# Kernel optimization log

Hardware: AMD Instinct MI355X
Metric: run time of the kernel (lower is better)

Reference implementation:

```python
import jax, jax.numpy as jnp
import numpy as np

EPS = 1e-5

def bn_relu(x, g, b):
    # MinkowskiBatchNorm (training mode: batch statistics over points) + ReLU
    mu = x.mean(0)
    var = jnp.var(x, axis=0)
    return jax.nn.relu((x - mu) * jax.lax.rsqrt(var + EPS) * g + b)

def setup_inputs() -> dict:
    key = jax.random.key(0)
    ks = jax.random.split(key, 8)
    N, C, H, K, M = 131072, 128, 2, 27, 2
    x = jax.random.normal(ks[0], (N, C), jnp.float32)
    nbr = jax.random.randint(ks[1], (N, K), 0, N, dtype=jnp.int32)  # kernel map
    Wv = jax.random.normal(ks[2], (C, C * H), jnp.float32) * 0.05   # 1x1 conv for v
    gv, bv = jnp.ones(C * H), jnp.zeros(C * H)
    Wq = jax.random.normal(ks[3], (K, C, 1), jnp.float32) * 0.05    # 3x3x3 conv for q (vec_dim=1)
    gq, bq = jnp.ones(1), jnp.zeros(1)
    cb = jax.random.normal(ks[4], (M, K, C * H), jnp.float32) * 0.05  # M channelwise conv kernels
    Wout = jax.random.normal(ks[5], (C * H, C), jnp.float32) * 0.05   # out 1x1 conv
    go, bo = jnp.ones(C), jnp.zeros(C)
    return dict(x=x, nbr=nbr, Wv=Wv, gv=gv, bv=bv, Wq=Wq, gq=gq, bq=bq,
                cb=cb, Wout=Wout, go=go, bo=bo)

def reference(x, nbr, Wv, gv, bv, Wq, gq, bq, cb, Wout, go, bo):
    N = x.shape[0]
    res = x  # inplanes == planes -> no downsample
    v = bn_relu(x @ Wv, gv, bv)                      # [N, 2C]
    nbrT = nbr.T                                     # [K, N]

    # q: sparse 3x3x3 conv planes -> vec_dim=1, scan over the 27 kernel offsets
    def qbody(acc, inp):
        idx, w = inp                                 # idx [N], w [C,1]
        return acc + x[idx] @ w, None
    q, _ = jax.lax.scan(qbody, jnp.zeros((N, Wq.shape[2]), x.dtype), (nbrT, Wq))
    q = bn_relu(q, gq, bq)                           # [N, 1]

    # choice: channelwise conv of channel-broadcast q with each codebook kernel,
    # summed over channels (vec_dim=1) -> equivalent to q_nbr @ kernel_channel_sums.
    # Codebook kernels have requires_grad=False in this path.
    ksum = jax.lax.stop_gradient(cb).sum(-1)         # [M, K]
    qn = q[:, 0][nbr]                                # [N, K]
    choice = jax.nn.softmax(qn @ ksum.T, axis=-1)    # [N, M], temp = 1

    # routed channelwise convs on v: sum_m choice[:,m] * chanconv_m(v)
    # fused as per-offset mix of the M kernels by choice.
    def obody(acc, inp):
        idx, wk = inp                                # idx [N], wk [M, 2C]
        return acc + v[idx] * (choice @ wk), None
    out, _ = jax.lax.scan(obody, jnp.zeros_like(v), (nbrT, jnp.swapaxes(cb, 0, 1)))

    out = bn_relu(out @ Wout, go, bo)                # [N, C]
    return out + res
```

## Files before the change

### kernel.cpp

```cpp
#include <hip/hip_runtime.h>
#include <math.h>

#define EPSV 1e-5f

__device__ __forceinline__ unsigned short f2bf(float f) {
    unsigned u = __float_as_uint(f);
    u += 0x7fffu + ((u >> 16) & 1u);
    return (unsigned short)(u >> 16);
}
__device__ __forceinline__ float bf2f(unsigned short h) {
    return __uint_as_float(((unsigned)h) << 16);
}

__global__ __launch_bounds__(256)
void prep_kernel(const float* __restrict__ Wv, const float* __restrict__ Wq,
                 const float* __restrict__ cb,
                 float* __restrict__ wcat, float* __restrict__ ksum,
                 float* __restrict__ stats)
{
    const long gid = (long)blockIdx.x * 256 + threadIdx.x;
    if (gid < 128L * 384) {
        const int r = (int)(gid / 384);
        const int c = (int)(gid % 384);
        float v = 0.f;
        if (c < 256)      v = Wv[r * 256 + c];
        else if (c < 283) v = Wq[(c - 256) * 128 + r];
        wcat[gid] = v;
    }
    if (gid < 1024) stats[gid] = 0.f;
    if (gid < 64) {
        float s = 0.f;
        if (gid < 27) { const float* p = cb + gid * 256; for (int c = 0; c < 256; ++c) s += p[c]; }
        else if (gid >= 32 && gid < 59) { const float* p = cb + (27 + (gid - 32)) * 256; for (int c = 0; c < 256; ++c) s += p[c]; }
        ksum[gid] = s;
    }
}

__global__ __launch_bounds__(256)
void gemm1_kernel(const float* __restrict__ A,
                  const float* __restrict__ B,
                  unsigned short* __restrict__ t1b,
                  float* __restrict__ y)
{
    __shared__ float As[16][132];
    __shared__ float Bs[16][132];
    const int tid = threadIdx.x;
    const int tx = tid & 15;
    const int ty = tid >> 4;
    const long rowBase = (long)blockIdx.y * 128;
    const int  colBase = blockIdx.x * 128;

    float acc[8][8];
    #pragma unroll
    for (int i = 0; i < 8; ++i)
        #pragma unroll
        for (int j = 0; j < 8; ++j) acc[i][j] = 0.f;

    const int ar = tid >> 2;
    const int ak = (tid & 3) * 4;
    const int bk = tid >> 5;
    const int bc = (tid & 31) * 4;

    for (int k0 = 0; k0 < 128; k0 += 16) {
        #pragma unroll
        for (int p = 0; p < 2; ++p) {
            const int r = ar + p * 64;
            const float4 av = *(const float4*)(A + (rowBase + r) * 128 + (k0 + ak));
            As[ak + 0][r] = av.x;
            As[ak + 1][r] = av.y;
            As[ak + 2][r] = av.z;
            As[ak + 3][r] = av.w;
        }
        #pragma unroll
        for (int p = 0; p < 2; ++p) {
            const int kk = bk + p * 8;
            *(float4*)&Bs[kk][bc] = *(const float4*)(B + (long)(k0 + kk) * 384 + (colBase + bc));
        }
        __syncthreads();
        #pragma unroll
        for (int kk = 0; kk < 16; ++kk) {
            const float4 a0 = *(const float4*)&As[kk][ty * 8];
            const float4 a1 = *(const float4*)&As[kk][ty * 8 + 4];
            const float4 b0 = *(const float4*)&Bs[kk][tx * 4];
            const float4 b1 = *(const float4*)&Bs[kk][64 + tx * 4];
            const float a[8] = {a0.x, a0.y, a0.z, a0.w, a1.x, a1.y, a1.z, a1.w};
            const float b[8] = {b0.x, b0.y, b0.z, b0.w, b1.x, b1.y, b1.z, b1.w};
            #pragma unroll
            for (int i = 0; i < 8; ++i)
                #pragma unroll
                for (int j = 0; j < 8; ++j)
                    acc[i][j] = fmaf(a[i], b[j], acc[i][j]);
        }
        __syncthreads();
    }

    if (colBase < 256) {
        #pragma unroll
        for (int i = 0; i < 8; ++i) {
            const long r = rowBase + ty * 8 + i;
            ushort4 u0, u1;
            u0.x = f2bf(acc[i][0]); u0.y = f2bf(acc[i][1]); u0.z = f2bf(acc[i][2]); u0.w = f2bf(acc[i][3]);
            u1.x = f2bf(acc[i][4]); u1.y = f2bf(acc[i][5]); u1.z = f2bf(acc[i][6]); u1.w = f2bf(acc[i][7]);
            *(ushort4*)(t1b + r * 256 + colBase + tx * 4)      = u0;
            *(ushort4*)(t1b + r * 256 + colBase + 64 + tx * 4) = u1;
        }
    } else {
        #pragma unroll
        for (int i = 0; i < 8; ++i) {
            const long r = rowBase + ty * 8 + i;
            #pragma unroll
            for (int j = 0; j < 8; ++j) {
                const int c = ((j < 4) ? (tx * 4 + j) : (64 + tx * 4 + (j - 4)));
                if (c < 27) y[r * 27 + c] = acc[i][j];
            }
        }
    }
}

__global__ __launch_bounds__(256)
void stats_t1(const unsigned short* __restrict__ t1b, float* __restrict__ stats)
{
    const int c = threadIdx.x;
    const long r0 = (long)blockIdx.x * 256;
    float s = 0.f, s2 = 0.f;
    #pragma unroll 4
    for (int r = 0; r < 256; ++r) {
        const float v = bf2f(t1b[(r0 + r) * 256 + c]);
        s += v; s2 += v * v;
    }
    atomicAdd(&stats[c], s);
    atomicAdd(&stats[256 + c], s2);
}

__global__ __launch_bounds__(256)
void qpre_kernel(const float* __restrict__ y, const int* __restrict__ nbr,
                 float* __restrict__ qpre, float* __restrict__ stats)
{
    __shared__ int snbr[256 * 27];
    __shared__ float red[8];
    const int tid = threadIdx.x;
    const long base = (long)blockIdx.x * 256;
    for (int j = tid; j < 256 * 27; j += 256) snbr[j] = nbr[base * 27 + j];
    __syncthreads();
    float q = 0.f;
    #pragma unroll
    for (int k = 0; k < 27; ++k) {
        const int idx = snbr[tid * 27 + k];
        q += y[(long)idx * 27 + k];
    }
    qpre[base + tid] = q;
    float s = q, s2 = q * q;
    #pragma unroll
    for (int off = 32; off > 0; off >>= 1) {
        s  += __shfl_xor(s, off);
        s2 += __shfl_xor(s2, off);
    }
    const int wid = tid >> 6;
    if ((tid & 63) == 0) { red[wid] = s; red[4 + wid] = s2; }
    __syncthreads();
    if (tid == 0) {
        atomicAdd(&stats[512], red[0] + red[1] + red[2] + red[3]);
        atomicAdd(&stats[513], red[4] + red[5] + red[6] + red[7]);
    }
}

__global__ __launch_bounds__(256, 4)
void gather_route(const unsigned short* __restrict__ t1b, const float* __restrict__ qpre,
                  const int* __restrict__ nbr, const float* __restrict__ cb,
                  const float* __restrict__ ksum, const float* __restrict__ stats,
                  const float* __restrict__ gv, const float* __restrict__ bvp,
                  const float* __restrict__ gq, const float* __restrict__ bq,
                  unsigned short* __restrict__ outpre, float inv_n)
{
    const long p  = (long)((blockIdx.x * 256 + threadIdx.x) >> 6);
    const int lane = threadIdx.x & 63;
    const int c4   = lane * 4;

    float a[4], b[4];
    #pragma unroll
    for (int j = 0; j < 4; ++j) {
        const float mu  = stats[c4 + j] * inv_n;
        const float var = stats[256 + c4 + j] * inv_n - mu * mu;
        const float sc  = gv[c4 + j] * rsqrtf(var + EPSV);
        a[j] = sc;
        b[j] = bvp[c4 + j] - mu * sc;
    }
    float s0 = 0.f, s1 = 0.f;
    int idx = 0;
    {
        const float muq  = stats[512] * inv_n;
        const float varq = stats[513] * inv_n - muq * muq;
        const float aq   = gq[0] * rsqrtf(varq + EPSV);
        const float bqc  = bq[0] - muq * aq;
        if (lane < 27) {
            idx = nbr[p * 27 + lane];
            const float qn = fmaxf(fmaf(qpre[idx], aq, bqc), 0.f);
            s0 = qn * ksum[lane];
            s1 = qn * ksum[32 + lane];
        }
    }
    #pragma unroll
    for (int off = 32; off > 0; off >>= 1) {
        s0 += __shfl_xor(s0, off);
        s1 += __shfl_xor(s1, off);
    }
    const float mm = fmaxf(s0, s1);
    const float e0 = __expf(s0 - mm);
    const float e1 = __expf(s1 - mm);
    const float c0 = e0 / (e0 + e1);
    const float c1 = 1.f - c0;

    float acc0[4] = {0, 0, 0, 0}, acc1[4] = {0, 0, 0, 0};
    #pragma unroll
    for (int k = 0; k < 27; ++k) {
        const int ik = __shfl(idx, k);
        const uint2 uu  = *(const uint2*)(t1b + (long)ik * 256 + c4);
        const float4 w0 = *(const float4*)(cb + k * 256 + c4);
        const float4 w1 = *(const float4*)(cb + (27 + k) * 256 + c4);
        const float t0 = __uint_as_float(uu.x << 16);
        const float t1v = __uint_as_float(uu.x & 0xffff0000u);
        const float t2v = __uint_as_float(uu.y << 16);
        const float t3 = __uint_as_float(uu.y & 0xffff0000u);
        const float v0 = fmaxf(fmaf(t0,  a[0], b[0]), 0.f);
        const float v1 = fmaxf(fmaf(t1v, a[1], b[1]), 0.f);
        const float v2 = fmaxf(fmaf(t2v, a[2], b[2]), 0.f);
        const float v3 = fmaxf(fmaf(t3,  a[3], b[3]), 0.f);
        acc0[0] = fmaf(v0, w0.x, acc0[0]); acc0[1] = fmaf(v1, w0.y, acc0[1]);
        acc0[2] = fmaf(v2, w0.z, acc0[2]); acc0[3] = fmaf(v3, w0.w, acc0[3]);
        acc1[0] = fmaf(v0, w1.x, acc1[0]); acc1[1] = fmaf(v1, w1.y, acc1[1]);
        acc1[2] = fmaf(v2, w1.z, acc1[2]); acc1[3] = fmaf(v3, w1.w, acc1[3]);
    }
    ushort4 o;
    o.x = f2bf(fmaf(c0, acc0[0], c1 * acc1[0]));
    o.y = f2bf(fmaf(c0, acc0[1], c1 * acc1[1]));
    o.z = f2bf(fmaf(c0, acc0[2], c1 * acc1[2]));
    o.w = f2bf(fmaf(c0, acc0[3], c1 * acc1[3]));
    *(ushort4*)(outpre + p * 256 + c4) = o;
}

__global__ __launch_bounds__(256)
void gemm2_kernel(const unsigned short* __restrict__ A,
                  const float* __restrict__ B,
                  float* __restrict__ C)
{
    __shared__ float As[16][132];
    __shared__ float Bs[16][132];
    const int tid = threadIdx.x;
    const int tx = tid & 15;
    const int ty = tid >> 4;
    const long rowBase = (long)blockIdx.x * 128;

    float acc[8][8];
    #pragma unroll
    for (int i = 0; i < 8; ++i)
        #pragma unroll
        for (int j = 0; j < 8; ++j) acc[i][j] = 0.f;

    const int ar = tid >> 1;
    const int ak = (tid & 1) * 8;
    const int bk = tid >> 5;
    const int bc = (tid & 31) * 4;

    for (int k0 = 0; k0 < 256; k0 += 16) {
        const uint4 av = *(const uint4*)(A + (rowBase + ar) * 256 + (k0 + ak));
        As[ak + 0][ar] = __uint_as_float(av.x << 16);
        As[ak + 1][ar] = __uint_as_float(av.x & 0xffff0000u);
        As[ak + 2][ar] = __uint_as_float(av.y << 16);
        As[ak + 3][ar] = __uint_as_float(av.y & 0xffff0000u);
        As[ak + 4][ar] = __uint_as_float(av.z << 16);
        As[ak + 5][ar] = __uint_as_float(av.z & 0xffff0000u);
        As[ak + 6][ar] = __uint_as_float(av.w << 16);
        As[ak + 7][ar] = __uint_as_float(av.w & 0xffff0000u);
        #pragma unroll
        for (int q = 0; q < 2; ++q) {
            const int kk = bk + q * 8;
            *(float4*)&Bs[kk][bc] = *(const float4*)(B + (long)(k0 + kk) * 128 + bc);
        }
        __syncthreads();
        #pragma unroll
        for (int kk = 0; kk < 16; ++kk) {
            const float4 a0 = *(const float4*)&As[kk][ty * 8];
            const float4 a1 = *(const float4*)&As[kk][ty * 8 + 4];
            const float4 b0 = *(const float4*)&Bs[kk][tx * 4];
            const float4 b1 = *(const float4*)&Bs[kk][64 + tx * 4];
            const float a[8] = {a0.x, a0.y, a0.z, a0.w, a1.x, a1.y, a1.z, a1.w};
            const float b[8] = {b0.x, b0.y, b0.z, b0.w, b1.x, b1.y, b1.z, b1.w};
            #pragma unroll
            for (int i = 0; i < 8; ++i)
                #pragma unroll
                for (int j = 0; j < 8; ++j)
                    acc[i][j] = fmaf(a[i], b[j], acc[i][j]);
        }
        __syncthreads();
    }
    #pragma unroll
    for (int i = 0; i < 8; ++i) {
        const long r = rowBase + ty * 8 + i;
        float4 o0 = make_float4(acc[i][0], acc[i][1], acc[i][2], acc[i][3]);
        float4 o1 = make_float4(acc[i][4], acc[i][5], acc[i][6], acc[i][7]);
        *(float4*)(C + r * 128 + tx * 4)      = o0;
        *(float4*)(C + r * 128 + 64 + tx * 4) = o1;
    }
}

__global__ __launch_bounds__(128)
void stats_t2(const float* __restrict__ t2, float* __restrict__ stats)
{
    const int c = threadIdx.x;
    const long r0 = (long)blockIdx.x * 128;
    float s = 0.f, s2 = 0.f;
    #pragma unroll 4
    for (int r = 0; r < 128; ++r) {
        const float v = t2[(r0 + r) * 128 + c];
        s += v; s2 += v * v;
    }
    atomicAdd(&stats[544 + c], s);
    atomicAdd(&stats[672 + c], s2);
}

__global__ __launch_bounds__(256)
void final_kernel(const float* __restrict__ t2, const float* __restrict__ x,
                  const float* __restrict__ stats,
                  const float* __restrict__ go, const float* __restrict__ bo,
                  float* __restrict__ out, long total4, float inv_n)
{
    const long i = (long)blockIdx.x * 256 + threadIdx.x;
    if (i >= total4) return;
    const int c4 = (int)((i * 4) & 127);
    float a[4], b[4];
    #pragma unroll
    for (int j = 0; j < 4; ++j) {
        const float mu  = stats[544 + c4 + j] * inv_n;
        const float var = stats[672 + c4 + j] * inv_n - mu * mu;
        const float sc  = go[c4 + j] * rsqrtf(var + EPSV);
        a[j] = sc;
        b[j] = bo[c4 + j] - mu * sc;
    }
    const float4 t  = *((const float4*)t2 + i);
    const float4 xx = *((const float4*)x + i);
    float4 o;
    o.x = fmaxf(fmaf(t.x, a[0], b[0]), 0.f) + xx.x;
    o.y = fmaxf(fmaf(t.y, a[1], b[1]), 0.f) + xx.y;
    o.z = fmaxf(fmaf(t.z, a[2], b[2]), 0.f) + xx.z;
    o.w = fmaxf(fmaf(t.w, a[3], b[3]), 0.f) + xx.w;
    *((float4*)out + i) = o;
}

extern "C" void kernel_launch(void* const* d_in, const int* in_sizes, int n_in,
                              void* d_out, int out_size, void* d_ws, size_t ws_size,
                              hipStream_t stream)
{
    const float* x    = (const float*)d_in[0];
    const int*   nbr  = (const int*)d_in[1];
    const float* Wv   = (const float*)d_in[2];
    const float* gv   = (const float*)d_in[3];
    const float* bv   = (const float*)d_in[4];
    const float* Wq   = (const float*)d_in[5];
    const float* gq   = (const float*)d_in[6];
    const float* bq   = (const float*)d_in[7];
    const float* cb   = (const float*)d_in[8];
    const float* Wout = (const float*)d_in[9];
    const float* go   = (const float*)d_in[10];
    const float* bo   = (const float*)d_in[11];
    float* out = (float*)d_out;
    float* ws  = (float*)d_ws;

    const int N = in_sizes[0] / 128;
    const float inv_n = 1.f / (float)N;

    float* wcat  = ws;
    float* ksum  = ws + 49152;
    float* stats = ws + 49216;
    unsigned short* t1b = (unsigned short*)(ws + 65536);
    float* y    = ws + 65536 + (long)N * 128;
    float* qpre = y + (long)N * 27;
    unsigned short* outpre = (unsigned short*)(qpre + N);
    float* t2   = out;

    hipLaunchKernelGGL(prep_kernel, dim3(192), dim3(256), 0, stream,
                       Wv, Wq, cb, wcat, ksum, stats);
    hipLaunchKernelGGL(gemm1_kernel, dim3(3, N / 128), dim3(256), 0, stream,
                       x, wcat, t1b, y);
    hipLaunchKernelGGL(stats_t1, dim3(N / 256), dim3(256), 0, stream, t1b, stats);
    hipLaunchKernelGGL(qpre_kernel, dim3(N / 256), dim3(256), 0, stream, y, nbr, qpre, stats);
    hipLaunchKernelGGL(gather_route, dim3(N / 4), dim3(256), 0, stream,
                       t1b, qpre, nbr, cb, ksum, stats, gv, bv, gq, bq, outpre, inv_n);
    hipLaunchKernelGGL(gemm2_kernel, dim3(N / 128), dim3(256), 0, stream,
                       outpre, Wout, t2);
    hipLaunchKernelGGL(stats_t2, dim3(N / 128), dim3(128), 0, stream, t2, stats);
    hipLaunchKernelGGL(final_kernel, dim3((unsigned)(((long)N * 128 / 4 + 255) / 256)), dim3(256), 0, stream,
                       t2, x, stats, go, bo, out, (long)N * 128 / 4, inv_n);
}
```

Baseline: 862.1 us.

## Prefetch all 27 neighbor rows upfront and interleave bf16 codebook weights

The gather_route kernel now issues all 27 neighbor-row loads into registers before computing the routing softmax, so the random gathers overlap with the softmax instead of being serialized inside the accumulate loop. The neighbor index is broadcast with readlane rather than shfl. The two codebook kernels are pre-interleaved into one bf16 buffer in the prep kernel, so each offset needs one 16-byte load instead of two float4 loads. The occupancy hint is dropped to allow the larger register footprint, which may lower occupancy, and the bf16 weights slightly reduce precision.

Measured after the change: 1.024 ms. 18.8% more time.

```diff
diff --git a/kernel.cpp b/kernel.cpp
--- a/kernel.cpp
+++ b/kernel.cpp
@@ -16,7 +16,7 @@
 void prep_kernel(const float* __restrict__ Wv, const float* __restrict__ Wq,
                  const float* __restrict__ cb,
                  float* __restrict__ wcat, float* __restrict__ ksum,
-                 float* __restrict__ stats)
+                 unsigned short* __restrict__ cbi, float* __restrict__ stats)
 {
     const long gid = (long)blockIdx.x * 256 + threadIdx.x;
     if (gid < 128L * 384) {
@@ -26,6 +26,15 @@
         if (c < 256)      v = Wv[r * 256 + c];
         else if (c < 283) v = Wq[(c - 256) * 128 + r];
         wcat[gid] = v;
+    }
+    if (gid < 27 * 512) {
+        const int k = (int)(gid >> 9);
+        const int r = (int)(gid & 511);
+        const int g = r >> 3;
+        const int h = r & 7;
+        const float v = (h < 4) ? cb[k * 256 + g * 4 + h]
+                                : cb[(27 + k) * 256 + g * 4 + (h - 4)];
+        cbi[gid] = f2bf(v);
     }
     if (gid < 1024) stats[gid] = 0.f;
     if (gid < 64) {
@@ -164,17 +173,27 @@
     }
 }
 
-__global__ __launch_bounds__(256, 4)
+__global__ __launch_bounds__(256)
 void gather_route(const unsigned short* __restrict__ t1b, const float* __restrict__ qpre,
-                  const int* __restrict__ nbr, const float* __restrict__ cb,
+                  const int* __restrict__ nbr, const unsigned short* __restrict__ cbi,
                   const float* __restrict__ ksum, const float* __restrict__ stats,
                   const float* __restrict__ gv, const float* __restrict__ bvp,
                   const float* __restrict__ gq, const float* __restrict__ bq,
                   unsigned short* __restrict__ outpre, float inv_n)
 {
-    const long p  = (long)((blockIdx.x * 256 + threadIdx.x) >> 6);
+    const long p   = (long)((blockIdx.x * 256 + threadIdx.x) >> 6);
     const int lane = threadIdx.x & 63;
     const int c4   = lane * 4;
+
+    int idx = 0;
+    if (lane < 27) idx = nbr[p * 27 + lane];
+
+    uint2 u[27];
+    #pragma unroll
+    for (int k = 0; k < 27; ++k) {
+        const int ik = __builtin_amdgcn_readlane(idx, k);
+        u[k] = *(const uint2*)(t1b + (long)ik * 256 + c4);
+    }
 
     float a[4], b[4];
     #pragma unroll
@@ -186,14 +205,12 @@
         b[j] = bvp[c4 + j] - mu * sc;
     }
     float s0 = 0.f, s1 = 0.f;
-    int idx = 0;
     {
         const float muq  = stats[512] * inv_n;
         const float varq = stats[513] * inv_n - muq * muq;
         const float aq   = gq[0] * rsqrtf(varq + EPSV);
         const float bqc  = bq[0] - muq * aq;
         if (lane < 27) {
-            idx = nbr[p * 27 + lane];
             const float qn = fmaxf(fmaf(qpre[idx], aq, bqc), 0.f);
             s0 = qn * ksum[lane];
             s1 = qn * ksum[32 + lane];
@@ -213,22 +230,27 @@
     float acc0[4] = {0, 0, 0, 0}, acc1[4] = {0, 0, 0, 0};
     #pragma unroll
     for (int k = 0; k < 27; ++k) {
-        const int ik = __shfl(idx, k);
-        const uint2 uu  = *(const uint2*)(t1b + (long)ik * 256 + c4);
-        const float4 w0 = *(const float4*)(cb + k * 256 + c4);
-        const float4 w1 = *(const float4*)(cb + (27 + k) * 256 + c4);
-        const float t0 = __uint_as_float(uu.x << 16);
-        const float t1v = __uint_as_float(uu.x & 0xffff0000u);
-        const float t2v = __uint_as_float(uu.y << 16);
-        const float t3 = __uint_as_float(uu.y & 0xffff0000u);
+        const uint4 w = *(const uint4*)(cbi + k * 512 + lane * 8);
+        const float t0  = __uint_as_float(u[k].x << 16);
+        const float t1v = __uint_as_float(u[k].x & 0xffff0000u);
+        const float t2v = __uint_as_float(u[k].y << 16);
+        const float t3  = __uint_as_float(u[k].y & 0xffff0000u);
         const float v0 = fmaxf(fmaf(t0,  a[0], b[0]), 0.f);
         const float v1 = fmaxf(fmaf(t1v, a[1], b[1]), 0.f);
         const float v2 = fmaxf(fmaf(t2v, a[2], b[2]), 0.f);
         const float v3 = fmaxf(fmaf(t3,  a[3], b[3]), 0.f);
-        acc0[0] = fmaf(v0, w0.x, acc0[0]); acc0[1] = fmaf(v1, w0.y, acc0[1]);
-        acc0[2] = fmaf(v2, w0.z, acc0[2]); acc0[3] = fmaf(v3, w0.w, acc0[3]);
-        acc1[0] = fmaf(v0, w1.x, acc1[0]); acc1[1] = fmaf(v1, w1.y, acc1[1]);
-        acc1[2] = fmaf(v2, w1.z, acc1[2]); acc1[3] = fmaf(v3, w1.w, acc1[3]);
+        const float w00 = __uint_as_float(w.x << 16);
+        const float w01 = __uint_as_float(w.x & 0xffff0000u);
+        const float w02 = __uint_as_float(w.y << 16);
+        const float w03 = __uint_as_float(w.y & 0xffff0000u);
+        const float w10 = __uint_as_float(w.z << 16);
+        const float w11 = __uint_as_float(w.z & 0xffff0000u);
+        const float w12 = __uint_as_float(w.w << 16);
+        const float w13 = __uint_as_float(w.w & 0xffff0000u);
+        acc0[0] = fmaf(v0, w00, acc0[0]); acc0[1] = fmaf(v1, w01, acc0[1]);
+        acc0[2] = fmaf(v2, w02, acc0[2]); acc0[3] = fmaf(v3, w03, acc0[3]);
+        acc1[0] = fmaf(v0, w10, acc1[0]); acc1[1] = fmaf(v1, w11, acc1[1]);
+        acc1[2] = fmaf(v2, w12, acc1[2]); acc1[3] = fmaf(v3, w13, acc1[3]);
     }
     ushort4 o;
     o.x = f2bf(fmaf(c0, acc0[0], c1 * acc1[0]));
@@ -371,6 +393,7 @@
     float* wcat  = ws;
     float* ksum  = ws + 49152;
     float* stats = ws + 49216;
+    unsigned short* cbi = (unsigned short*)(ws + 50240);
     unsigned short* t1b = (unsigned short*)(ws + 65536);
     float* y    = ws + 65536 + (long)N * 128;
     float* qpre = y + (long)N * 27;
@@ -378,13 +401,13 @@
     float* t2   = out;
 
     hipLaunchKernelGGL(prep_kernel, dim3(192), dim3(256), 0, stream,
-                       Wv, Wq, cb, wcat, ksum, stats);
+                       Wv, Wq, cb, wcat, ksum, cbi, stats);
     hipLaunchKernelGGL(gemm1_kernel, dim3(3, N / 128), dim3(256), 0, stream,
                        x, wcat, t1b, y);
     hipLaunchKernelGGL(stats_t1, dim3(N / 256), dim3(256), 0, stream, t1b, stats);
     hipLaunchKernelGGL(qpre_kernel, dim3(N / 256), dim3(256), 0, stream, y, nbr, qpre, stats);
     hipLaunchKernelGGL(gather_route, dim3(N / 4), dim3(256), 0, stream,
-                       t1b, qpre, nbr, cb, ksum, stats, gv, bv, gq, bq, outpre, inv_n);
+                       t1b, qpre, nbr, cbi, ksum, stats, gv, bv, gq, bq, outpre, inv_n);
     hipLaunchKernelGGL(gemm2_kernel, dim3(N / 128), dim3(256), 0, stream,
                        outpre, Wout, t2);
     hipLaunchKernelGGL(stats_t2, dim3(N / 128), dim3(128), 0, stream, t2, stats);
```

## Replace FP32 SIMT GEMMs with bf16 MFMA kernels and pre-packed weights

Applied to the files above, without the earlier changes.

Both dense projections (x@Wv and out@Wout) now use a templated bf16 MFMA 16x16x32 kernel. The weights are pre-packed into fragment layout in the prep kernel. The q projection gets its own MFMA kernel that splits operands into hi and lo bf16 parts, keeping near-fp32 accuracy for the sensitive routing scores. The codebook in the gather kernel is interleaved and stored as bf16 so one 16-byte load per offset fetches both mixing kernels. The aim is to move the GEMM FLOPs off scalar FMAs onto matrix cores, at the cost of reduced precision in the v and output projections.

Result: slower. 1.667 ms (+93.4%).

```diff
diff --git a/kernel.cpp b/kernel.cpp
--- a/kernel.cpp
+++ b/kernel.cpp
@@ -2,6 +2,9 @@
 #include <math.h>
 
 #define EPSV 1e-5f
+
+typedef __attribute__((ext_vector_type(8))) short bf16x8;
+typedef __attribute__((ext_vector_type(4))) float f32x4;
 
 __device__ __forceinline__ unsigned short f2bf(float f) {
     unsigned u = __float_as_uint(f);
@@ -14,18 +17,51 @@
 
 __global__ __launch_bounds__(256)
 void prep_kernel(const float* __restrict__ Wv, const float* __restrict__ Wq,
-                 const float* __restrict__ cb,
-                 float* __restrict__ wcat, float* __restrict__ ksum,
+                 const float* __restrict__ cb, const float* __restrict__ Wout,
+                 float* __restrict__ ksum, unsigned short* __restrict__ cbi,
+                 unsigned short* __restrict__ Bvp, unsigned short* __restrict__ Bop,
+                 unsigned short* __restrict__ Bqh, unsigned short* __restrict__ Bql,
                  float* __restrict__ stats)
 {
     const long gid = (long)blockIdx.x * 256 + threadIdx.x;
-    if (gid < 128L * 384) {
-        const int r = (int)(gid / 384);
-        const int c = (int)(gid % 384);
-        float v = 0.f;
-        if (c < 256)      v = Wv[r * 256 + c];
-        else if (c < 283) v = Wq[(c - 256) * 128 + r];
-        wcat[gid] = v;
+    if (gid < 27 * 512) {
+        const int k = (int)(gid >> 9);
+        const int r = (int)(gid & 511);
+        const int g = r >> 3;
+        const int h = r & 7;
+        const float v = (h < 4) ? cb[k * 256 + g * 4 + h]
+                                : cb[(27 + k) * 256 + g * 4 + (h - 4)];
+        cbi[gid] = f2bf(v);
+    }
+    if (gid < 32768) {
+        const int i = (int)(gid & 7);
+        const int l = (int)((gid >> 3) & 63);
+        const int rest = (int)(gid >> 9);
+        const int ks = rest & 3, nf = rest >> 2;
+        const int k = ks * 32 + ((l >> 4) << 3) + i;
+        const int n = nf * 16 + (l & 15);
+        Bvp[gid] = f2bf(Wv[k * 256 + n]);
+    }
+    if (gid < 32768) {
+        const int i = (int)(gid & 7);
+        const int l = (int)((gid >> 3) & 63);
+        const int rest = (int)(gid >> 9);
+        const int ks = rest & 7, nf = rest >> 3;
+        const int k = ks * 32 + ((l >> 4) << 3) + i;
+        const int n = nf * 16 + (l & 15);
+        Bop[gid] = f2bf(Wout[k * 128 + n]);
+    }
+    if (gid < 4096) {
+        const int i = (int)(gid & 7);
+        const int l = (int)((gid >> 3) & 63);
+        const int rest = (int)(gid >> 9);
+        const int ks = rest & 3, nf = rest >> 2;
+        const int k = ks * 32 + ((l >> 4) << 3) + i;
+        const int n = nf * 16 + (l & 15);
+        const float w = (n < 27) ? Wq[n * 128 + k] : 0.f;
+        const unsigned short h = f2bf(w);
+        Bqh[gid] = h;
+        Bql[gid] = f2bf(w - bf2f(h));
     }
     if (gid < 1024) stats[gid] = 0.f;
     if (gid < 64) {
@@ -36,85 +72,146 @@
     }
 }
 
-__global__ __launch_bounds__(256)
-void gemm1_kernel(const float* __restrict__ A,
-                  const float* __restrict__ B,
-                  unsigned short* __restrict__ t1b,
-                  float* __restrict__ y)
-{
-    __shared__ float As[16][132];
-    __shared__ float Bs[16][132];
-    const int tid = threadIdx.x;
-    const int tx = tid & 15;
-    const int ty = tid >> 4;
-    const long rowBase = (long)blockIdx.y * 128;
-    const int  colBase = blockIdx.x * 128;
-
-    float acc[8][8];
-    #pragma unroll
-    for (int i = 0; i < 8; ++i)
-        #pragma unroll
-        for (int j = 0; j < 8; ++j) acc[i][j] = 0.f;
-
-    const int ar = tid >> 2;
-    const int ak = (tid & 3) * 4;
-    const int bk = tid >> 5;
-    const int bc = (tid & 31) * 4;
-
-    for (int k0 = 0; k0 < 128; k0 += 16) {
-        #pragma unroll
-        for (int p = 0; p < 2; ++p) {
-            const int r = ar + p * 64;
-            const float4 av = *(const float4*)(A + (rowBase + r) * 128 + (k0 + ak));
-            As[ak + 0][r] = av.x;
-            As[ak + 1][r] = av.y;
-            As[ak + 2][r] = av.z;
-            As[ak + 3][r] = av.w;
-        }
-        #pragma unroll
-        for (int p = 0; p < 2; ++p) {
-            const int kk = bk + p * 8;
-            *(float4*)&Bs[kk][bc] = *(const float4*)(B + (long)(k0 + kk) * 384 + (colBase + bc));
+template<int K, bool ABF, bool OUTBF>
+__global__ __launch_bounds__(256)
+void mfma_gemm(const void* __restrict__ Avoid, const unsigned short* __restrict__ Bp,
+               unsigned short* __restrict__ Cb, float* __restrict__ Cf, int ldc)
+{
+    __shared__ unsigned short As[128][40];
+    const int tid  = threadIdx.x;
+    const int w    = tid >> 6, lane = tid & 63;
+    const int r15  = lane & 15, g = lane >> 4;
+    const long m0  = (long)blockIdx.y * 128;
+    const int n0   = blockIdx.x * 64;
+    const int nfrag0 = n0 >> 4;
+    const int srow = tid >> 1;
+    const int shalf = tid & 1;
+
+    f32x4 acc[2][4];
+    #pragma unroll
+    for (int a_ = 0; a_ < 2; ++a_)
+        #pragma unroll
+        for (int b_ = 0; b_ < 4; ++b_) acc[a_][b_] = (f32x4){0.f, 0.f, 0.f, 0.f};
+
+    for (int ks = 0; ks < K / 32; ++ks) {
+        const int k0 = ks * 32;
+        __syncthreads();
+        if constexpr (ABF) {
+            const unsigned short* A = (const unsigned short*)Avoid;
+            const uint4 v0 = *(const uint4*)(A + (m0 + srow) * K + k0 + shalf * 16);
+            const uint4 v1 = *(const uint4*)(A + (m0 + srow) * K + k0 + shalf * 16 + 8);
+            *(uint4*)&As[srow][shalf * 16]     = v0;
+            *(uint4*)&As[srow][shalf * 16 + 8] = v1;
+        } else {
+            const float* A = (const float*)Avoid + (m0 + srow) * K + k0 + shalf * 16;
+            const float4 f0 = *(const float4*)(A + 0);
+            const float4 f1 = *(const float4*)(A + 4);
+            const float4 f2 = *(const float4*)(A + 8);
+            const float4 f3 = *(const float4*)(A + 12);
+            ushort4 h0 = { f2bf(f0.x), f2bf(f0.y), f2bf(f0.z), f2bf(f0.w) };
+            ushort4 h1 = { f2bf(f1.x), f2bf(f1.y), f2bf(f1.z), f2bf(f1.w) };
+            ushort4 h2 = { f2bf(f2.x), f2bf(f2.y), f2bf(f2.z), f2bf(f2.w) };
+            ushort4 h3 = { f2bf(f3.x), f2bf(f3.y), f2bf(f3.z), f2bf(f3.w) };
+            *(ushort4*)&As[srow][shalf * 16 + 0]  = h0;
+            *(ushort4*)&As[srow][shalf * 16 + 4]  = h1;
+            *(ushort4*)&As[srow][shalf * 16 + 8]  = h2;
+            *(ushort4*)&As[srow][shalf * 16 + 12] = h3;
         }
         __syncthreads();
-        #pragma unroll
-        for (int kk = 0; kk < 16; ++kk) {
-            const float4 a0 = *(const float4*)&As[kk][ty * 8];
-            const float4 a1 = *(const float4*)&As[kk][ty * 8 + 4];
-            const float4 b0 = *(const float4*)&Bs[kk][tx * 4];
-            const float4 b1 = *(const float4*)&Bs[kk][64 + tx * 4];
-            const float a[8] = {a0.x, a0.y, a0.z, a0.w, a1.x, a1.y, a1.z, a1.w};
-            const float b[8] = {b0.x, b0.y, b0.z, b0.w, b1.x, b1.y, b1.z, b1.w};
+        bf16x8 af0 = *(const bf16x8*)&As[w * 32 + r15][g * 8];
+        bf16x8 af1 = *(const bf16x8*)&As[w * 32 + 16 + r15][g * 8];
+        #pragma unroll
+        for (int nf = 0; nf < 4; ++nf) {
+            const bf16x8 bf = *(const bf16x8*)(Bp + (((nfrag0 + nf) * (K / 32) + ks) * 64 + lane) * 8);
+            acc[0][nf] = __builtin_amdgcn_mfma_f32_16x16x32_bf16(af0, bf, acc[0][nf], 0, 0, 0);
+            acc[1][nf] = __builtin_amdgcn_mfma_f32_16x16x32_bf16(af1, bf, acc[1][nf], 0, 0, 0);
+        }
+    }
+    #pragma unroll
+    for (int fr = 0; fr < 2; ++fr)
+        #pragma unroll
+        for (int nf = 0; nf < 4; ++nf)
             #pragma unroll
-            for (int i = 0; i < 8; ++i)
-                #pragma unroll
-                for (int j = 0; j < 8; ++j)
-                    acc[i][j] = fmaf(a[i], b[j], acc[i][j]);
+            for (int r = 0; r < 4; ++r) {
+                const long row = m0 + w * 32 + fr * 16 + g * 4 + r;
+                const int col = n0 + nf * 16 + r15;
+                if constexpr (OUTBF) Cb[row * ldc + col] = f2bf(acc[fr][nf][r]);
+                else                 Cf[row * ldc + col] = acc[fr][nf][r];
+            }
+}
+
+__global__ __launch_bounds__(256)
+void mfma_y(const float* __restrict__ X, const unsigned short* __restrict__ Bqh,
+            const unsigned short* __restrict__ Bql, float* __restrict__ y)
+{
+    __shared__ unsigned short Ah[128][40];
+    __shared__ unsigned short Al[128][40];
+    const int tid  = threadIdx.x;
+    const int w    = tid >> 6, lane = tid & 63;
+    const int r15  = lane & 15, g = lane >> 4;
+    const long m0  = (long)blockIdx.y * 128;
+    const int srow = tid >> 1;
+    const int shalf = tid & 1;
+
+    f32x4 acc[2][2];
+    #pragma unroll
+    for (int a_ = 0; a_ < 2; ++a_)
+        #pragma unroll
+        for (int b_ = 0; b_ < 2; ++b_) acc[a_][b_] = (f32x4){0.f, 0.f, 0.f, 0.f};
+
+    for (int ks = 0; ks < 4; ++ks) {
+        const int k0 = ks * 32;
+        __syncthreads();
+        {
+            const float* A = X + (m0 + srow) * 128 + k0 + shalf * 16;
+            float fs[16];
+            const float4 f0 = *(const float4*)(A + 0);
+            const float4 f1 = *(const float4*)(A + 4);
+            const float4 f2 = *(const float4*)(A + 8);
+            const float4 f3 = *(const float4*)(A + 12);
+            fs[0]=f0.x; fs[1]=f0.y; fs[2]=f0.z; fs[3]=f0.w;
+            fs[4]=f1.x; fs[5]=f1.y; fs[6]=f1.z; fs[7]=f1.w;
+            fs[8]=f2.x; fs[9]=f2.y; fs[10]=f2.z; fs[11]=f2.w;
+            fs[12]=f3.x; fs[13]=f3.y; fs[14]=f3.z; fs[15]=f3.w;
+            #pragma unroll
+            for (int q4 = 0; q4 < 4; ++q4) {
+                ushort4 hq, lq;
+                unsigned short h;
+                h = f2bf(fs[q4*4+0]); hq.x = h; lq.x = f2bf(fs[q4*4+0] - bf2f(h));
+                h = f2bf(fs[q4*4+1]); hq.y = h; lq.y = f2bf(fs[q4*4+1] - bf2f(h));
+                h = f2bf(fs[q4*4+2]); hq.z = h; lq.z = f2bf(fs[q4*4+2] - bf2f(h));
+                h = f2bf(fs[q4*4+3]); hq.w = h; lq.w = f2bf(fs[q4*4+3] - bf2f(h));
+                *(ushort4*)&Ah[srow][shalf * 16 + q4 * 4] = hq;
+                *(ushort4*)&Al[srow][shalf * 16 + q4 * 4] = lq;
+            }
         }
         __syncthreads();
-    }
-
-    if (colBase < 256) {
-        #pragma unroll
-        for (int i = 0; i < 8; ++i) {
-            const long r = rowBase + ty * 8 + i;
-            ushort4 u0, u1;
-            u0.x = f2bf(acc[i][0]); u0.y = f2bf(acc[i][1]); u0.z = f2bf(acc[i][2]); u0.w = f2bf(acc[i][3]);
-            u1.x = f2bf(acc[i][4]); u1.y = f2bf(acc[i][5]); u1.z = f2bf(acc[i][6]); u1.w = f2bf(acc[i][7]);
-            *(ushort4*)(t1b + r * 256 + colBase + tx * 4)      = u0;
-            *(ushort4*)(t1b + r * 256 + colBase + 64 + tx * 4) = u1;
+        bf16x8 ah0 = *(const bf16x8*)&Ah[w * 32 + r15][g * 8];
+        bf16x8 ah1 = *(const bf16x8*)&Ah[w * 32 + 16 + r15][g * 8];
+        bf16x8 al0 = *(const bf16x8*)&Al[w * 32 + r15][g * 8];
+        bf16x8 al1 = *(const bf16x8*)&Al[w * 32 + 16 + r15][g * 8];
+        #pragma unroll
+        for (int nf = 0; nf < 2; ++nf) {
+            const bf16x8 bh = *(const bf16x8*)(Bqh + ((nf * 4 + ks) * 64 + lane) * 8);
+            const bf16x8 bl = *(const bf16x8*)(Bql + ((nf * 4 + ks) * 64 + lane) * 8);
+            acc[0][nf] = __builtin_amdgcn_mfma_f32_16x16x32_bf16(ah0, bh, acc[0][nf], 0, 0, 0);
+            acc[0][nf] = __builtin_amdgcn_mfma_f32_16x16x32_bf16(ah0, bl, acc[0][nf], 0, 0, 0);
+            acc[0][nf] = __builtin_amdgcn_mfma_f32_16x16x32_bf16(al0, bh, acc[0][nf], 0, 0, 0);
+            acc[1][nf] = __builtin_amdgcn_mfma_f32_16x16x32_bf16(ah1, bh, acc[1][nf], 0, 0, 0);
+            acc[1][nf] = __builtin_amdgcn_mfma_f32_16x16x32_bf16(ah1, bl, acc[1][nf], 0, 0, 0);
+            acc[1][nf] = __builtin_amdgcn_mfma_f32_16x16x32_bf16(al1, bh, acc[1][nf], 0, 0, 0);
         }
-    } else {
-        #pragma unroll
-        for (int i = 0; i < 8; ++i) {
-            const long r = rowBase + ty * 8 + i;
+    }
+    #pragma unroll
+    for (int fr = 0; fr < 2; ++fr)
+        #pragma unroll
+        for (int nf = 0; nf < 2; ++nf)
             #pragma unroll
-            for (int j = 0; j < 8; ++j) {
-                const int c = ((j < 4) ? (tx * 4 + j) : (64 + tx * 4 + (j - 4)));
-                if (c < 27) y[r * 27 + c] = acc[i][j];
+            for (int r = 0; r < 4; ++r) {
+                const long row = m0 + w * 32 + fr * 16 + g * 4 + r;
+                const int col = nf * 16 + r15;
+                if (col < 27) y[row * 27 + col] = acc[fr][nf][r];
             }
-        }
-    }
 }
 
 __global__ __launch_bounds__(256)
@@ -166,13 +263,13 @@
 
 __global__ __launch_bounds__(256, 4)
 void gather_route(const unsigned short* __restrict__ t1b, const float* __restrict__ qpre,
-                  const int* __restrict__ nbr, const float* __restrict__ cb,
+                  const int* __restrict__ nbr, const unsigned short* __restrict__ cbi,
                   const float* __restrict__ ksum, const float* __restrict__ stats,
                   const float* __restrict__ gv, const float* __restrict__ bvp,
                   const float* __restrict__ gq, const float* __restrict__ bq,
                   unsigned short* __restrict__ outpre, float inv_n)
 {
-    const long p  = (long)((blockIdx.x * 256 + threadIdx.x) >> 6);
+    const long p   = (long)((blockIdx.x * 256 + threadIdx.x) >> 6);
     const int lane = threadIdx.x & 63;
     const int c4   = lane * 4;
 
@@ -214,21 +311,24 @@
     #pragma unroll
     for (int k = 0; k < 27; ++k) {
         const int ik = __shfl(idx, k);
-        const uint2 uu  = *(const uint2*)(t1b + (long)ik * 256 + c4);
-        const float4 w0 = *(const float4*)(cb + k * 256 + c4);
-        const float4 w1 = *(const float4*)(cb + (27 + k) * 256 + c4);
-        const float t0 = __uint_as_float(uu.x << 16);
+        const uint2 uu = *(const uint2*)(t1b + (long)ik * 256 + c4);
+        const uint4 w  = *(const uint4*)(cbi + k * 512 + lane * 8);
+        const float t0  = __uint_as_float(uu.x << 16);
         const float t1v = __uint_as_float(uu.x & 0xffff0000u);
         const float t2v = __uint_as_float(uu.y << 16);
-        const float t3 = __uint_as_float(uu.y & 0xffff0000u);
+        const float t3  = __uint_as_float(uu.y & 0xffff0000u);
         const float v0 = fmaxf(fmaf(t0,  a[0], b[0]), 0.f);
         const float v1 = fmaxf(fmaf(t1v, a[1], b[1]), 0.f);
         const float v2 = fmaxf(fmaf(t2v, a[2], b[2]), 0.f);
         const float v3 = fmaxf(fmaf(t3,  a[3], b[3]), 0.f);
-        acc0[0] = fmaf(v0, w0.x, acc0[0]); acc0[1] = fmaf(v1, w0.y, acc0[1]);
-        acc0[2] = fmaf(v2, w0.z, acc0[2]); acc0[3] = fmaf(v3, w0.w, acc0[3]);
-        acc1[0] = fmaf(v0, w1.x, acc1[0]); acc1[1] = fmaf(v1, w1.y, acc1[1]);
-        acc1[2] = fmaf(v2, w1.z, acc1[2]); acc1[3] = fmaf(v3, w1.w, acc1[3]);
+        acc0[0] = fmaf(v0, __uint_as_float(w.x << 16),         acc0[0]);
+        acc0[1] = fmaf(v1, __uint_as_float(w.x & 0xffff0000u), acc0[1]);
+        acc0[2] = fmaf(v2, __uint_as_float(w.y << 16),         acc0[2]);
+        acc0[3] = fmaf(v3, __uint_as_float(w.y & 0xffff0000u), acc0[3]);
+        acc1[0] = fmaf(v0, __uint_as_float(w.z << 16),         acc1[0]);
+        acc1[1] = fmaf(v1, __uint_as_float(w.z & 0xffff0000u), acc1[1]);
+        acc1[2] = fmaf(v2, __uint_as_float(w.w << 16),         acc1[2]);
+        acc1[3] = fmaf(v3, __uint_as_float(w.w & 0xffff0000u), acc1[3]);
     }
     ushort4 o;
     o.x = f2bf(fmaf(c0, acc0[0], c1 * acc1[0]));
@@ -236,71 +336,6 @@
     o.z = f2bf(fmaf(c0, acc0[2], c1 * acc1[2]));
     o.w = f2bf(fmaf(c0, acc0[3], c1 * acc1[3]));
     *(ushort4*)(outpre + p * 256 + c4) = o;
-}
-
-__global__ __launch_bounds__(256)
-void gemm2_kernel(const unsigned short* __restrict__ A,
-                  const float* __restrict__ B,
-                  float* __restrict__ C)
-{
-    __shared__ float As[16][132];
-    __shared__ float Bs[16][132];
-    const int tid = threadIdx.x;
-    const int tx = tid & 15;
-    const int ty = tid >> 4;
-    const long rowBase = (long)blockIdx.x * 128;
-
-    float acc[8][8];
-    #pragma unroll
-    for (int i = 0; i < 8; ++i)
-        #pragma unroll
-        for (int j = 0; j < 8; ++j) acc[i][j] = 0.f;
-
-    const int ar = tid >> 1;
-    const int ak = (tid & 1) * 8;
-    const int bk = tid >> 5;
-    const int bc = (tid & 31) * 4;
-
-    for (int k0 = 0; k0 < 256; k0 += 16) {
-        const uint4 av = *(const uint4*)(A + (rowBase + ar) * 256 + (k0 + ak));
-        As[ak + 0][ar] = __uint_as_float(av.x << 16);
-        As[ak + 1][ar] = __uint_as_float(av.x & 0xffff0000u);
-        As[ak + 2][ar] = __uint_as_float(av.y << 16);
-        As[ak + 3][ar] = __uint_as_float(av.y & 0xffff0000u);
-        As[ak + 4][ar] = __uint_as_float(av.z << 16);
-        As[ak + 5][ar] = __uint_as_float(av.z & 0xffff0000u);
-        As[ak + 6][ar] = __uint_as_float(av.w << 16);
-        As[ak + 7][ar] = __uint_as_float(av.w & 0xffff0000u);
-        #pragma unroll
-        for (int q = 0; q < 2; ++q) {
-            const int kk = bk + q * 8;
-            *(float4*)&Bs[kk][bc] = *(const float4*)(B + (long)(k0 + kk) * 128 + bc);
-        }
-        __syncthreads();
-        #pragma unroll
-        for (int kk = 0; kk < 16; ++kk) {
-            const float4 a0 = *(const float4*)&As[kk][ty * 8];
-            const float4 a1 = *(const float4*)&As[kk][ty * 8 + 4];
-            const float4 b0 = *(const float4*)&Bs[kk][tx * 4];
-            const float4 b1 = *(const float4*)&Bs[kk][64 + tx * 4];
-            const float a[8] = {a0.x, a0.y, a0.z, a0.w, a1.x, a1.y, a1.z, a1.w};
-            const float b[8] = {b0.x, b0.y, b0.z, b0.w, b1.x, b1.y, b1.z, b1.w};
-            #pragma unroll
-            for (int i = 0; i < 8; ++i)
-                #pragma unroll
-                for (int j = 0; j < 8; ++j)
-                    acc[i][j] = fmaf(a[i], b[j], acc[i][j]);
-        }
-        __syncthreads();
-    }
-    #pragma unroll
-    for (int i = 0; i < 8; ++i) {
-        const long r = rowBase + ty * 8 + i;
-        float4 o0 = make_float4(acc[i][0], acc[i][1], acc[i][2], acc[i][3]);
-        float4 o1 = make_float4(acc[i][4], acc[i][5], acc[i][6], acc[i][7]);
-        *(float4*)(C + r * 128 + tx * 4)      = o0;
-        *(float4*)(C + r * 128 + 64 + tx * 4) = o1;
-    }
 }
 
 __global__ __launch_bounds__(128)
@@ -368,9 +403,13 @@
     const int N = in_sizes[0] / 128;
     const float inv_n = 1.f / (float)N;
 
-    float* wcat  = ws;
-    float* ksum  = ws + 49152;
-    float* stats = ws + 49216;
+    float* ksum  = ws;
+    float* stats = ws + 64;
+    unsigned short* cbi = (unsigned short*)(ws + 2048);
+    unsigned short* Bvp = (unsigned short*)(ws + 9216);
+    unsigned short* Bop = (unsigned short*)(ws + 25600);
+    unsigned short* Bqh = (unsigned short*)(ws + 41984);
+    unsigned short* Bql = (unsigned short*)(ws + 44032);
     unsigned short* t1b = (unsigned short*)(ws + 65536);
     float* y    = ws + 65536 + (long)N * 128;
     float* qpre = y + (long)N * 27;
@@ -378,15 +417,16 @@
     float* t2   = out;
 
     hipLaunchKernelGGL(prep_kernel, dim3(192), dim3(256), 0, stream,
-                       Wv, Wq, cb, wcat, ksum, stats);
-    hipLaunchKernelGGL(gemm1_kernel, dim3(3, N / 128), dim3(256), 0, stream,
-                       x, wcat, t1b, y);
+                       Wv, Wq, cb, Wout, ksum, cbi, Bvp, Bop, Bqh, Bql, stats);
+    mfma_gemm<128, false, true><<<dim3(4, N / 128), dim3(256), 0, stream>>>(
+        (const void*)x, Bvp, t1b, (float*)nullptr, 256);
+    mfma_y<<<dim3(1, N / 128), dim3(256), 0, stream>>>(x, Bqh, Bql, y);
     hipLaunchKernelGGL(stats_t1, dim3(N / 256), dim3(256), 0, stream, t1b, stats);
     hipLaunchKernelGGL(qpre_kernel, dim3(N / 256), dim3(256), 0, stream, y, nbr, qpre, stats);
     hipLaunchKernelGGL(gather_route, dim3(N / 4), dim3(256), 0, stream,
-                       t1b, qpre, nbr, cb, ksum, stats, gv, bv, gq, bq, outpre, inv_n);
-    hipLaunchKernelGGL(gemm2_kernel, dim3(N / 128), dim3(256), 0, stream,
-                       outpre, Wout, t2);
+                       t1b, qpre, nbr, cbi, ksum, stats, gv, bv, gq, bq, outpre, inv_n);
+    mfma_gemm<256, true, false><<<dim3(2, N / 128), dim3(256), 0, stream>>>(
+        (const void*)outpre, Bop, (unsigned short*)nullptr, t2, 128);
     hipLaunchKernelGGL(stats_t2, dim3(N / 128), dim3(128), 0, stream, t2, stats);
     hipLaunchKernelGGL(final_kernel, dim3((unsigned)(((long)N * 128 / 4 + 255) / 256)), dim3(256), 0, stream,
                        t2, x, stats, go, bo, out, (long)N * 128 / 4, inv_n);
```
